# Performance work log

Measured on AMD Instinct MI355X. Metric: run time of the kernel, lower is better.

## Reference

```python
import jax, jax.numpy as jnp
from jax import lax
import numpy as np

MIN_VAL = -100000.0
B, T, NUM_TAGS = 512, 1024, 126
K = NUM_TAGS + 2  # augmented with START (index -1) and END (index -2)


def setup_inputs() -> dict:
    key = jax.random.key(0)
    k1, k2 = jax.random.split(key)
    feats = jax.random.normal(k1, (B, T, K), dtype=jnp.float32)
    trans = 0.1 * jax.random.normal(k2, (K, K), dtype=jnp.float32)
    # replicate original init constraints: no transition INTO START, none FROM END
    trans = trans.at[K - 1, :].set(MIN_VAL)  # START_TAG == -1
    trans = trans.at[:, K - 2].set(MIN_VAL)  # END_TAG == -2
    return {"feats": feats, "trans": trans}


def reference(feats, trans):
    """Batched linear-chain CRF forward algorithm (log partition function).

    feats: [B, T, K] emission scores (K = num_tags + 2, last two are END, START)
    trans: [K, K]    trans[to, frm] transition scores
    returns: [B] log Z per sequence
    """
    b, t, k = feats.shape
    START, END = k - 1, k - 2
    init_alpha = jnp.full((b, k), MIN_VAL, dtype=feats.dtype).at[:, START].set(0.0)

    def step(alpha, feat_t):  # alpha: [B,K], feat_t: [B,K]
        # scores[b, to, frm] = trans[to, frm] + alpha[b, frm]
        scores = trans[None, :, :] + alpha[:, None, :]
        new_alpha = jax.nn.logsumexp(scores, axis=-1) + feat_t
        return new_alpha, None

    feats_tm = jnp.swapaxes(feats, 0, 1)  # [T, B, K], time-major for scan
    alpha, _ = lax.scan(step, init_alpha, feats_tm)
    final = alpha + trans[END][None, :]
    return jax.nn.logsumexp(final, axis=-1)  # [B]
```

## Files before the change

### kernel.cpp

```cpp
#include <hip/hip_runtime.h>
#include <hip/hip_bf16.h>
#include <math.h>

#define TT 1024
#define KK 128
#define BB 512
#define TPB 256
#define MINV -100000.0f

typedef float v2f __attribute__((ext_vector_type(2)));

__device__ __forceinline__ int padidx(int f) { return f + ((f >> 4) << 2); }

__global__ __launch_bounds__(TPB, 2)
void crf_fwd_kernel(const float* __restrict__ feats,
                    const float* __restrict__ trans,
                    float* __restrict__ out)
{
    const int b    = blockIdx.x;
    const int tid  = threadIdx.x;
    const int g    = tid >> 3;
    const int o    = tid & 7;
    const int rr   = ((o & 1) << 1) | ((o >> 1) & 1);
    const int to_out = (g << 2) + rr;
    const int lane = tid & 63;
    const int wv   = tid >> 6;

    __shared__ __align__(16) float p_lds[2][160];
    __shared__ float mslot[2];
    __shared__ float wred[4];
    __shared__ float sred[4];

    v2f E2[4][8];
    #pragma unroll
    for (int r = 0; r < 4; ++r) {
        const float4* tr = reinterpret_cast<const float4*>(trans + (g * 4 + r) * KK + o * 16);
        #pragma unroll
        for (int i = 0; i < 4; ++i) {
            float4 v = tr[i];
            E2[r][2 * i + 0] = v2f{__expf(v.x), __expf(v.y)};
            E2[r][2 * i + 1] = v2f{__expf(v.z), __expf(v.w)};
        }
    }
    const float tEnd = trans[(KK - 2) * KK + to_out];

    const float* fp = feats + (size_t)b * TT * KK + to_out;
    float f0 = fp[0];
    float f1 = fp[KK];
    fp += 2 * KK;

    float a = (to_out == KK - 1) ? 0.0f : MINV;
    float m = 0.0f;

    for (int t = 0; t < TT; ++t) {
        const int buf = t & 1;

        float f2 = 0.0f;
        if (t + 2 < TT) f2 = *fp;
        fp += KK;

        if (tid == 0) mslot[buf] = a;
        const float pv = __expf(a - m);
        if (o < 4) p_lds[buf][padidx(to_out)] = pv;
        __syncthreads();

        const float m_next = (t == 0) ? 0.0f : mslot[buf];

        const float* pbase = &p_lds[buf][o * 20];
        v2f acc0 = {0.f,0.f}, acc1 = {0.f,0.f}, acc2 = {0.f,0.f}, acc3 = {0.f,0.f};
        #pragma unroll
        for (int i = 0; i < 4; ++i) {
            float4 pq = *reinterpret_cast<const float4*>(pbase + i * 4);
            v2f plo = v2f{pq.x, pq.y};
            v2f phi = v2f{pq.z, pq.w};
            acc0 = __builtin_elementwise_fma(E2[0][2 * i], plo, acc0);
            acc1 = __builtin_elementwise_fma(E2[1][2 * i], plo, acc1);
            acc2 = __builtin_elementwise_fma(E2[2][2 * i], plo, acc2);
            acc3 = __builtin_elementwise_fma(E2[3][2 * i], plo, acc3);
            acc0 = __builtin_elementwise_fma(E2[0][2 * i + 1], phi, acc0);
            acc1 = __builtin_elementwise_fma(E2[1][2 * i + 1], phi, acc1);
            acc2 = __builtin_elementwise_fma(E2[2][2 * i + 1], phi, acc2);
            acc3 = __builtin_elementwise_fma(E2[3][2 * i + 1], phi, acc3);
        }
        float s0 = acc0.x + acc0.y;
        float s1 = acc1.x + acc1.y;
        float s2 = acc2.x + acc2.y;
        float s3 = acc3.x + acc3.y;

        float send_lo = (o & 1) ? s0 : s2;
        float send_hi = (o & 1) ? s1 : s3;
        float recv_lo = __shfl_xor(send_lo, 1, 64);
        float recv_hi = __shfl_xor(send_hi, 1, 64);
        float qa = ((o & 1) ? s2 : s0) + recv_lo;
        float qb = ((o & 1) ? s3 : s1) + recv_hi;
        float send2 = (o & 2) ? qa : qb;
        float recv2 = __shfl_xor(send2, 2, 64);
        float sv = ((o & 2) ? qb : qa) + recv2;
        sv += __shfl_xor(sv, 4, 64);

        a = __logf(sv) + m + f0;
        f0 = f1; f1 = f2;
        m = m_next;
    }

    const float fin = a + tEnd;
    float wm = fin;
    #pragma unroll
    for (int s = 32; s >= 1; s >>= 1)
        wm = fmaxf(wm, __shfl_xor(wm, s, 64));
    if (lane == 0) wred[wv] = wm;
    __syncthreads();
    float M = fmaxf(fmaxf(wred[0], wred[1]), fmaxf(wred[2], wred[3]));

    float e = (o < 4) ? __expf(fin - M) : 0.0f;
    #pragma unroll
    for (int s = 32; s >= 1; s >>= 1)
        e += __shfl_xor(e, s, 64);
    if (lane == 0) sred[wv] = e;
    __syncthreads();
    if (tid == 0)
        out[b] = M + __logf(((sred[0] + sred[1]) + (sred[2] + sred[3])));
}

extern "C" void kernel_launch(void* const* d_in, const int* in_sizes, int n_in,
                              void* d_out, int out_size, void* d_ws, size_t ws_size,
                              hipStream_t stream) {
    const float* feats = (const float*)d_in[0];
    const float* trans = (const float*)d_in[1];
    float* out = (float*)d_out;

    crf_fwd_kernel<<<BB, TPB, 0, stream>>>(feats, trans, out);
}
```

Baseline: 475.6 us.

## Run CRF recursion in scaled linear domain with DPP lane exchanges

Replaces the per-step log/exp recursion with a linear-domain recursion. Each step multiplies by exp(feat) and rescales by the reciprocal of tag-0's value, and the log of the scale is accumulated in a running sum. This removes the per-step exp of alpha and the log on the critical path. Cross-lane reductions switch from ds_bpermute shuffles to DPP moves, with lanes remapped so partners fall within DPP rows. The risk is underflow or overflow, since the scale is taken from a single tag rather than the maximum.

```diff
diff --git a/kernel.cpp b/kernel.cpp
--- a/kernel.cpp
+++ b/kernel.cpp
@@ -6,11 +6,21 @@
 #define KK 128
 #define BB 512
 #define TPB 256
-#define MINV -100000.0f
 
 typedef float v2f __attribute__((ext_vector_type(2)));
 
 __device__ __forceinline__ int padidx(int f) { return f + ((f >> 4) << 2); }
+
+template <int CTRL>
+__device__ __forceinline__ float dppf(float x) {
+    union { float f; int i; } u, o;
+    u.f = x;
+    o.i = __builtin_amdgcn_update_dpp(0, u.i, CTRL, 0xF, 0xF, false);
+    return o.f;
+}
+#define DPP_XOR1 0xB1
+#define DPP_XOR2 0x4E
+#define DPP_XOR8 0x128
 
 __global__ __launch_bounds__(TPB, 2)
 void crf_fwd_kernel(const float* __restrict__ feats,
@@ -19,16 +29,16 @@
 {
     const int b    = blockIdx.x;
     const int tid  = threadIdx.x;
-    const int g    = tid >> 3;
-    const int o    = tid & 7;
+    const int lane = tid & 63;
+    const int wave = tid >> 6;
+    const int o    = (lane & 3) | (((lane >> 3) & 1) << 2);
+    const int g    = ((lane >> 2) & 1) | (((lane >> 4) & 3) << 1) | (wave << 3);
     const int rr   = ((o & 1) << 1) | ((o >> 1) & 1);
-    const int to_out = (g << 2) + rr;
-    const int lane = tid & 63;
-    const int wv   = tid >> 6;
+    const int tag  = (g << 2) + rr;
+    const bool wr  = (o & 4) == 0;
 
-    __shared__ __align__(16) float p_lds[2][160];
-    __shared__ float mslot[2];
-    __shared__ float wred[4];
+    __shared__ __align__(16) float v_lds[2][160];
+    __shared__ float rslot[2];
     __shared__ float sred[4];
 
     v2f E2[4][8];
@@ -42,31 +52,32 @@
             E2[r][2 * i + 1] = v2f{__expf(v.z), __expf(v.w)};
         }
     }
-    const float tEnd = trans[(KK - 2) * KK + to_out];
+    const float eEnd = __expf(trans[(KK - 2) * KK + tag]);
 
-    const float* fp = feats + (size_t)b * TT * KK + to_out;
+    const float* fp = feats + (size_t)b * TT * KK + tag;
     float f0 = fp[0];
-    float f1 = fp[KK];
+    float fA = fp[KK];
     fp += 2 * KK;
+    float ef = __expf(f0);
 
-    float a = (to_out == KK - 1) ? 0.0f : MINV;
-    float m = 0.0f;
+    if (tid == 0) rslot[0] = 1.0f;
+    if (wr) v_lds[0][padidx(tag)] = (tag == KK - 1) ? 1.0f : 0.0f;
+    __syncthreads();
+
+    float La = 0.0f;
+    float vv = 0.0f;
 
     for (int t = 0; t < TT; ++t) {
         const int buf = t & 1;
 
-        float f2 = 0.0f;
-        if (t + 2 < TT) f2 = *fp;
+        float fC = 0.0f;
+        if (t + 2 < TT) fC = *fp;
         fp += KK;
+        const float ef_next = __expf(fA);
 
-        if (tid == 0) mslot[buf] = a;
-        const float pv = __expf(a - m);
-        if (o < 4) p_lds[buf][padidx(to_out)] = pv;
-        __syncthreads();
+        const float r = rslot[buf];
 
-        const float m_next = (t == 0) ? 0.0f : mslot[buf];
-
-        const float* pbase = &p_lds[buf][o * 20];
+        const float* pbase = &v_lds[buf][o * 20];
         v2f acc0 = {0.f,0.f}, acc1 = {0.f,0.f}, acc2 = {0.f,0.f}, acc3 = {0.f,0.f};
         #pragma unroll
         for (int i = 0; i < 4; ++i) {
@@ -89,37 +100,35 @@
 
         float send_lo = (o & 1) ? s0 : s2;
         float send_hi = (o & 1) ? s1 : s3;
-        float recv_lo = __shfl_xor(send_lo, 1, 64);
-        float recv_hi = __shfl_xor(send_hi, 1, 64);
+        float recv_lo = dppf<DPP_XOR1>(send_lo);
+        float recv_hi = dppf<DPP_XOR1>(send_hi);
         float qa = ((o & 1) ? s2 : s0) + recv_lo;
         float qb = ((o & 1) ? s3 : s1) + recv_hi;
         float send2 = (o & 2) ? qa : qb;
-        float recv2 = __shfl_xor(send2, 2, 64);
+        float recv2 = dppf<DPP_XOR2>(send2);
         float sv = ((o & 2) ? qb : qa) + recv2;
-        sv += __shfl_xor(sv, 4, 64);
+        sv += dppf<DPP_XOR8>(sv);
 
-        a = __logf(sv) + m + f0;
-        f0 = f1; f1 = f2;
-        m = m_next;
+        vv = sv * ef * r;
+        La -= __logf(r);
+
+        if (tid == 0) rslot[buf ^ 1] = __builtin_amdgcn_rcpf(vv);
+        if (wr) v_lds[buf ^ 1][padidx(tag)] = vv;
+
+        __syncthreads();
+
+        ef = ef_next;
+        fA = fC;
     }
 
-    const float fin = a + tEnd;
-    float wm = fin;
-    #pragma unroll
-    for (int s = 32; s >= 1; s >>= 1)
-        wm = fmaxf(wm, __shfl_xor(wm, s, 64));
-    if (lane == 0) wred[wv] = wm;
-    __syncthreads();
-    float M = fmaxf(fmaxf(wred[0], wred[1]), fmaxf(wred[2], wred[3]));
-
-    float e = (o < 4) ? __expf(fin - M) : 0.0f;
+    float e = wr ? vv * eEnd : 0.0f;
     #pragma unroll
     for (int s = 32; s >= 1; s >>= 1)
         e += __shfl_xor(e, s, 64);
-    if (lane == 0) sred[wv] = e;
+    if (lane == 0) sred[wave] = e;
     __syncthreads();
     if (tid == 0)
-        out[b] = M + __logf(((sred[0] + sred[1]) + (sred[2] + sred[3])));
+        out[b] = La + __logf((sred[0] + sred[1]) + (sred[2] + sred[3]));
 }
 
 extern "C" void kernel_launch(void* const* d_in, const int* in_sizes, int n_in,
```

Result: faster. 382.7 us (-19.5%).
